# Performance work log

Hardware: AMD Instinct MI355X
Metric: run time of the kernel (lower is better)

Reference implementation:

```python
import jax, jax.numpy as jnp
import numpy as np

N_ITEMS = 1_000_000
DIM = 32
B = 16384
N_KS = 50


def _make_table(key):
    # Spatial coords small, then project to hyperboloid: x0 = sqrt(1 + ||x_{1:}||^2)
    spatial = 0.001 * jax.random.uniform(key, (N_ITEMS + 1, DIM - 1), minval=-1.0, maxval=1.0)
    dim0 = jnp.sqrt(1.0 + jnp.sum(spatial ** 2, axis=1, keepdims=True))
    return jnp.concatenate([dim0, spatial], axis=1).astype(jnp.float32)


def setup_inputs() -> dict:
    key = jax.random.key(0)
    k1, k2, k3 = jax.random.split(key, 3)
    table = _make_table(k1)
    I = jax.random.randint(k2, (B,), 0, N_ITEMS)
    Ks = jax.random.randint(k3, (B, N_KS), 0, N_ITEMS)
    return {"table": table, "I": I, "Ks": Ks}


def reference(table, I, Ks):
    ui = table[I]                      # (B, D) anchor embeddings
    uks = table[Ks]                    # (B, N, D) positive + negatives
    m = ui[:, None, :] * uks           # broadcast over N (torch stacked copies)
    # Lorentz scalar product: sum of spatial parts minus time part
    lsp = jnp.sum(m[..., 1:], axis=-1) - m[..., 0]   # (B, N)
    d = -lsp
    d = jnp.where(d <= 1.0, jnp.float32(1.0 + 1e-6), d)
    d = -jnp.log(d + jnp.sqrt(d * d - 1.0))          # -arcosh(d)
    loss = -(d[:, 0] - jnp.log(jnp.sum(jnp.exp(d), axis=1) + 1e-6))
    return loss
```

## Files before the change

### kernel.cpp

```cpp
#include <hip/hip_runtime.h>

constexpr int DIM = 32;
constexpr int NKS = 50;

__global__ __launch_bounds__(256)
void lorentz_loss_kernel(const float* __restrict__ table,
                         const int* __restrict__ I,
                         const int* __restrict__ Ks,
                         float* __restrict__ out, int B)
{
    const int lane8 = threadIdx.x & 7;
    const int group = threadIdx.x >> 3;
    const int b     = blockIdx.x * 32 + group;
    if (b >= B) return;

    const float4* __restrict__ tab4 = reinterpret_cast<const float4*>(table);

    const long long i0 = I[b];
    const float4 u = tab4[i0 * (DIM / 4) + lane8];

    float4 us;
    us.x = (lane8 == 0) ? u.x : -u.x;
    us.y = -u.y;
    us.z = -u.z;
    us.w = -u.w;

    const int* __restrict__ ks = Ks + (long long)b * NKS;

    float d0 = 0.0f;
    float sumexp = 0.0f;

#pragma unroll 5
    for (int n = 0; n < NKS; ++n) {
        const long long k = ks[n];
        const float4 v4 = tab4[k * (DIM / 4) + lane8];

        float p = us.x * v4.x + us.y * v4.y + us.z * v4.z + us.w * v4.w;
        p += __shfl_xor(p, 4, 8);
        p += __shfl_xor(p, 2, 8);
        p += __shfl_xor(p, 1, 8);

        float dd  = (p <= 1.0f) ? 1.000001f : p;
        float arc = -logf(dd + sqrtf(dd * dd - 1.0f));

        d0 = (n == 0) ? arc : d0;
        sumexp += expf(arc);
    }

    if (lane8 == 0)
        out[b] = -(d0 - logf(sumexp + 1e-6f));
}

extern "C" void kernel_launch(void* const* d_in, const int* in_sizes, int n_in,
                              void* d_out, int out_size, void* d_ws, size_t ws_size,
                              hipStream_t stream) {
    const float* table = (const float*)d_in[0];
    const int*   I     = (const int*)d_in[1];
    const int*   Ks    = (const int*)d_in[2];
    float*       out   = (float*)d_out;

    const int B = in_sizes[1];
    const int blocks = (B + 31) / 32;

    lorentz_loss_kernel<<<blocks, 256, 0, stream>>>(table, I, Ks, out, B);
}
```

Before: 24.45 us.

## Assign one wavefront per batch row and replace log/exp with reciprocal

Each 64-lane wavefront now handles one batch row: eight 8-lane groups each process a strided subset of the 50 candidates, with Ks indices loaded cooperatively and broadcast via shuffles. The exp(-log(t)) per candidate is replaced algebraically by a hardware reciprocal of t, and the anchor term by log(t0), removing the transcendental calls. The goal is more independent gathers in flight per row and less serialized latency, at the cost of four rows per block, a cross-group shuffle reduction, and slightly different rounding from the approximate reciprocal.

```diff
diff --git a/kernel.cpp b/kernel.cpp
--- a/kernel.cpp
+++ b/kernel.cpp
@@ -9,15 +9,16 @@
                          const int* __restrict__ Ks,
                          float* __restrict__ out, int B)
 {
-    const int lane8 = threadIdx.x & 7;
-    const int group = threadIdx.x >> 3;
-    const int b     = blockIdx.x * 32 + group;
+    const int lane  = threadIdx.x & 63;
+    const int lane8 = lane & 7;
+    const int group = lane >> 3;
+    const int b     = blockIdx.x * 4 + (threadIdx.x >> 6);
     if (b >= B) return;
 
     const float4* __restrict__ tab4 = reinterpret_cast<const float4*>(table);
 
-    const long long i0 = I[b];
-    const float4 u = tab4[i0 * (DIM / 4) + lane8];
+    const int i0 = I[b];
+    const float4 u = tab4[(long long)i0 * 8 + lane8];
 
     float4 us;
     us.x = (lane8 == 0) ? u.x : -u.x;
@@ -25,30 +26,37 @@
     us.z = -u.z;
     us.w = -u.w;
 
-    const int* __restrict__ ks = Ks + (long long)b * NKS;
+    const int n_pre = group + 8 * lane8;
+    const int kn = (n_pre < NKS) ? Ks[(long long)b * NKS + n_pre] : 0;
 
-    float d0 = 0.0f;
-    float sumexp = 0.0f;
+    float sum = 0.0f;
+    float t0  = 1.0f;
 
-#pragma unroll 5
-    for (int n = 0; n < NKS; ++n) {
-        const long long k = ks[n];
-        const float4 v4 = tab4[k * (DIM / 4) + lane8];
+#pragma unroll
+    for (int t = 0; t < 7; ++t) {
+        const int n = group + 8 * t;
+        if (n < NKS) {
+            const int k = __shfl(kn, t, 8);
+            const float4 v = tab4[(long long)k * 8 + lane8];
 
-        float p = us.x * v4.x + us.y * v4.y + us.z * v4.z + us.w * v4.w;
-        p += __shfl_xor(p, 4, 8);
-        p += __shfl_xor(p, 2, 8);
-        p += __shfl_xor(p, 1, 8);
+            float p = us.x * v.x + us.y * v.y + us.z * v.z + us.w * v.w;
+            p += __shfl_xor(p, 4, 8);
+            p += __shfl_xor(p, 2, 8);
+            p += __shfl_xor(p, 1, 8);
 
-        float dd  = (p <= 1.0f) ? 1.000001f : p;
-        float arc = -logf(dd + sqrtf(dd * dd - 1.0f));
-
-        d0 = (n == 0) ? arc : d0;
-        sumexp += expf(arc);
+            const float dd = (p <= 1.0f) ? 1.000001f : p;
+            const float tt = dd + sqrtf(dd * dd - 1.0f);
+            sum += __builtin_amdgcn_rcpf(tt);
+            if (n == 0) t0 = tt;
+        }
     }
 
-    if (lane8 == 0)
-        out[b] = -(d0 - logf(sumexp + 1e-6f));
+    sum += __shfl_xor(sum, 8);
+    sum += __shfl_xor(sum, 16);
+    sum += __shfl_xor(sum, 32);
+
+    if (lane == 0)
+        out[b] = logf(t0) + logf(sum + 1e-6f);
 }
 
 extern "C" void kernel_launch(void* const* d_in, const int* in_sizes, int n_in,
@@ -60,7 +68,7 @@
     float*       out   = (float*)d_out;
 
     const int B = in_sizes[1];
-    const int blocks = (B + 31) / 32;
+    const int blocks = (B + 3) / 4;
 
     lorentz_loss_kernel<<<blocks, 256, 0, stream>>>(table, I, Ks, out, B);
 }
```

After: 24.25 us. Within noise of the previous version (-0.8%).
